# Kernel optimization log

Measured on AMD Instinct MI355X. Metric: run time of the kernel, lower is better.

The kernel has to match this reference:

```python
import jax, jax.numpy as jnp
import numpy as np

N, E, G = 16384, 131072, 64
IN_DIM, HID, HEADS, GDIM, OUT_DIM = 256, 128, 4, 2, 2


def _glorot(key, shape):
    fan_in = shape[0]
    return jax.random.normal(key, shape, dtype=jnp.float32) / jnp.sqrt(jnp.float32(fan_in))


def gatv2_layer(x, src, dst, Wl, bl, Wr, br, att, bias, heads, ch, concat):
    """GATv2Conv: e_ij = att . leaky_relu(Wl x_j + Wr x_i, 0.2), segment softmax over dst."""
    n = x.shape[0]
    xl = (x @ Wl + bl).reshape(n, heads, ch)  # source transform
    xr = (x @ Wr + br).reshape(n, heads, ch)  # target transform
    h = jax.nn.leaky_relu(xl[src] + xr[dst], 0.2)          # [E', H, C]
    e = jnp.einsum('ehc,hc->eh', h, att)                   # [E', H]
    m = jax.ops.segment_max(e, dst, num_segments=n)        # stable softmax per target
    p = jnp.exp(e - m[dst])
    denom = jax.ops.segment_sum(p, dst, num_segments=n)
    alpha = p / denom[dst]                                 # self-loops guarantee denom>0
    out = jax.ops.segment_sum(alpha[..., None] * xl[src], dst, num_segments=n)  # [n,H,C]
    out = out.reshape(n, heads * ch) if concat else out.mean(axis=1)
    return out + bias


def setup_inputs() -> dict:
    key = jax.random.key(0)
    ks = jax.random.split(key, 24)
    inp = {
        'x': jax.random.normal(ks[0], (N, IN_DIM), dtype=jnp.float32),
        'edge_index': jax.random.randint(ks[1], (2, E), 0, N, dtype=jnp.int64)
            if jax.config.jax_enable_x64 else jax.random.randint(ks[1], (2, E), 0, N).astype(jnp.int32),
        'batch': jnp.sort(jax.random.randint(ks[2], (N,), 0, G)).astype(jnp.int32),
        'global_features': jax.random.normal(ks[3], (G, GDIM), dtype=jnp.float32),
    }
    # conv1: in=256 -> heads*hid=512 (concat)
    inp['c1_Wl'] = _glorot(ks[4], (IN_DIM, HEADS * HID)); inp['c1_bl'] = jnp.zeros((HEADS * HID,), jnp.float32)
    inp['c1_Wr'] = _glorot(ks[5], (IN_DIM, HEADS * HID)); inp['c1_br'] = jnp.zeros((HEADS * HID,), jnp.float32)
    inp['c1_att'] = _glorot(ks[6], (HEADS, HID)); inp['c1_bias'] = jnp.zeros((HEADS * HID,), jnp.float32)
    # conv2: in=512 -> 512 (concat)
    D2 = HEADS * HID
    inp['c2_Wl'] = _glorot(ks[7], (D2, HEADS * HID)); inp['c2_bl'] = jnp.zeros((HEADS * HID,), jnp.float32)
    inp['c2_Wr'] = _glorot(ks[8], (D2, HEADS * HID)); inp['c2_br'] = jnp.zeros((HEADS * HID,), jnp.float32)
    inp['c2_att'] = _glorot(ks[9], (HEADS, HID)); inp['c2_bias'] = jnp.zeros((HEADS * HID,), jnp.float32)
    # conv3: in=512 -> 128 (heads=1, concat=False)
    inp['c3_Wl'] = _glorot(ks[10], (D2, HID)); inp['c3_bl'] = jnp.zeros((HID,), jnp.float32)
    inp['c3_Wr'] = _glorot(ks[11], (D2, HID)); inp['c3_br'] = jnp.zeros((HID,), jnp.float32)
    inp['c3_att'] = _glorot(ks[12], (1, HID)); inp['c3_bias'] = jnp.zeros((HID,), jnp.float32)
    # classifier: (hid + global_dim) -> hid -> out
    inp['cls_W1'] = _glorot(ks[13], (HID + GDIM, HID)); inp['cls_b1'] = jnp.zeros((HID,), jnp.float32)
    inp['cls_W2'] = _glorot(ks[14], (HID, OUT_DIM)); inp['cls_b2'] = jnp.zeros((OUT_DIM,), jnp.float32)
    return inp


def reference(x, edge_index, batch, global_features,
              c1_Wl, c1_bl, c1_Wr, c1_br, c1_att, c1_bias,
              c2_Wl, c2_bl, c2_Wr, c2_br, c2_att, c2_bias,
              c3_Wl, c3_bl, c3_Wr, c3_br, c3_att, c3_bias,
              cls_W1, cls_b1, cls_W2, cls_b2):
    n = x.shape[0]
    # PyG GATv2Conv add_self_loops=True default
    loop = jnp.arange(n, dtype=edge_index.dtype)
    src = jnp.concatenate([edge_index[0], loop])
    dst = jnp.concatenate([edge_index[1], loop])

    h = jax.nn.leaky_relu(gatv2_layer(x, src, dst, c1_Wl, c1_bl, c1_Wr, c1_br, c1_att, c1_bias, HEADS, HID, True), 0.01)
    h = jax.nn.leaky_relu(gatv2_layer(h, src, dst, c2_Wl, c2_bl, c2_Wr, c2_br, c2_att, c2_bias, HEADS, HID, True), 0.01)
    h = jax.nn.leaky_relu(gatv2_layer(h, src, dst, c3_Wl, c3_bl, c3_Wr, c3_br, c3_att, c3_bias, 1, HID, False), 0.01)

    # global mean pool over graphs
    counts = jax.ops.segment_sum(jnp.ones((n,), h.dtype), batch, num_segments=G)
    pooled = jax.ops.segment_sum(h, batch, num_segments=G) / jnp.maximum(counts, 1.0)[:, None]

    z = jnp.concatenate([pooled, global_features.reshape(G, -1)], axis=-1)
    z = jax.nn.leaky_relu(z @ cls_W1 + cls_b1, 0.01)  # Dropout is identity at eval
    return z @ cls_W2 + cls_b2
```

## Files before the change

kernel.cpp:

```cpp
#include <hip/hip_runtime.h>

typedef _Float16 h16;
typedef _Float16 h16x8 __attribute__((ext_vector_type(8)));
typedef float    f32x4 __attribute__((ext_vector_type(4)));

#define ELLW 40

__device__ __forceinline__ void gload16(const h16* g, h16* l) {
    __builtin_amdgcn_global_load_lds(
        (const __attribute__((address_space(1))) void*)g,
        (__attribute__((address_space(3))) void*)l,
        16, 0, 0);
}

__global__ __launch_bounds__(256) void prep(
    const float* __restrict__ W0, const float* __restrict__ W1,
    const float* __restrict__ W2, const float* __restrict__ W3,
    const float* __restrict__ W4, const float* __restrict__ W5,
    h16* __restrict__ O0, h16* __restrict__ O1, h16* __restrict__ O2,
    h16* __restrict__ O3, h16* __restrict__ O4, h16* __restrict__ O5,
    const float* __restrict__ x, h16* __restrict__ xh,
    int* __restrict__ cursor,
    const int* __restrict__ batch, int* __restrict__ start,
    float* __restrict__ pooled, int Nn, int G)
{
    __shared__ float lds[32][33];
    const int b = blockIdx.x;
    if (b < 896) {
        int mtx, t0;
        if      (b < 128) { mtx = 0; t0 = 0;   }
        else if (b < 256) { mtx = 1; t0 = 128; }
        else if (b < 512) { mtx = 2; t0 = 256; }
        else if (b < 768) { mtx = 3; t0 = 512; }
        else if (b < 832) { mtx = 4; t0 = 768; }
        else              { mtx = 5; t0 = 832; }
        const float* Ws[6] = {W0, W1, W2, W3, W4, W5};
        h16*         Os[6] = {O0, O1, O2, O3, O4, O5};
        const int    Ks[6] = {256, 256, 512, 512, 512, 512};
        const int    Ns[6] = {512, 512, 512, 512, 128, 128};
        const float* W = Ws[mtx];
        h16*         O = Os[mtx];
        const int K = Ks[mtx], N = Ns[mtx];
        const int tile = b - t0;
        const int tk = tile / (N >> 5), tn = tile % (N >> 5);
        const int t = threadIdx.x;
        const int r = t >> 3, c4 = (t & 7) * 4;
        float4 v = *(const float4*)(W + (size_t)(tk * 32 + r) * N + tn * 32 + c4);
        lds[r][c4] = v.x; lds[r][c4 + 1] = v.y; lds[r][c4 + 2] = v.z; lds[r][c4 + 3] = v.w;
        __syncthreads();
        h16* po = O + (size_t)(tn * 32 + r) * K + tk * 32 + c4;
        po[0] = (h16)lds[c4 + 0][r];
        po[1] = (h16)lds[c4 + 1][r];
        po[2] = (h16)lds[c4 + 2][r];
        po[3] = (h16)lds[c4 + 3][r];
        return;
    }
    int i = (b - 896) * 256 + threadIdx.x;
    const int n_x = Nn * 32;
    if (i < n_x) {
        float4 a = *(const float4*)(x + (size_t)i * 8);
        float4 c = *(const float4*)(x + (size_t)i * 8 + 4);
        h16x8 o = { (h16)a.x, (h16)a.y, (h16)a.z, (h16)a.w,
                    (h16)c.x, (h16)c.y, (h16)c.z, (h16)c.w };
        *(h16x8*)(xh + (size_t)i * 8) = o;
        return;
    }
    i -= n_x;
    if (i < Nn) { cursor[i] = 0; return; }
    i -= Nn;
    if (i < G * 128) { pooled[i] = 0.f; return; }
    i -= G * 128;
    if (i < Nn) {
        int bb = batch[i];
        int bp = (i == 0) ? -1 : batch[i - 1];
        for (int g = bp + 1; g <= bb; g++) start[g] = i;
        if (i == Nn - 1) for (int g = bb + 1; g <= G; g++) start[g] = Nn;
    }
}

__global__ void scatter_ell(const int* __restrict__ ei, int E, int Nn,
                            int* __restrict__ cursor, int* __restrict__ ssrc) {
    int i = blockIdx.x * blockDim.x + threadIdx.x;
    if (i >= E + Nn) return;
    int src, dst;
    if (i < E) { src = ei[i]; dst = ei[E + i]; }
    else       { src = dst = i - E; }
    int p = atomicAdd(&cursor[dst], 1);
    if (p < ELLW) ssrc[dst * ELLW + p] = src;
}

__device__ __forceinline__ void xcd_tiles(int& mt, int& nt) {
    int d = blockIdx.x + blockIdx.y * gridDim.x;
    int k = d & 7, j = d >> 3;
    mt = k * (gridDim.y >> 3) + j / gridDim.x;
    nt = j % gridDim.x;
}

__global__ __launch_bounds__(512) void gemm_f16_wide(
    const h16* __restrict__ Xh, const h16* __restrict__ Wt,
    const float* __restrict__ bias_lo, const float* __restrict__ bias_hi, int nsplit,
    h16* __restrict__ Yl, h16* __restrict__ Yr, int M, int N, int K)
{
    __shared__ __align__(16) h16 As[2][128 * 64];
    __shared__ __align__(16) h16 Bs[2][256 * 64];

    int mt, nt;
    xcd_tiles(mt, nt);
    const int m0 = mt * 128;
    const int n0 = nt * 256;
    const int t = threadIdx.x;
    const int lane = t & 63;
    const int wid = t >> 6;
    const int wr = wid >> 2;
    const int wc = wid & 3;

    f32x4 acc[4][4] = {};

    const int lr = lane >> 3;
    const int sl = lane & 7;

    #define STAGE(b, k0)                                                          \
        _Pragma("unroll")                                                         \
        for (int q = 0; q < 6; q++) {                                             \
            int rb = wid + 8 * q;                                                 \
            if (rb < 16) {                                                        \
                int r = rb * 8 + lr;                                              \
                int col = (sl ^ (r & 7)) << 3;                                    \
                gload16(Xh + (size_t)(m0 + r) * K + (k0) + col, &As[b][rb * 8 * 64]); \
            } else {                                                              \
                int c = (rb - 16) * 8 + lr;                                       \
                int col = (sl ^ (c & 7)) << 3;                                    \
                gload16(Wt + (size_t)(n0 + c) * K + (k0) + col, &Bs[b][(rb - 16) * 8 * 64]); \
            }                                                                     \
        }

    STAGE(0, 0)
    __syncthreads();

    const int nkb = K >> 6;
    int buf = 0;
    for (int kb = 0; kb < nkb; kb++) {
        if (kb + 1 < nkb) { STAGE(buf ^ 1, (kb + 1) << 6) }
        #pragma unroll
        for (int ks = 0; ks < 2; ks++) {
            h16x8 af[4], bf[4];
            #pragma unroll
            for (int i = 0; i < 4; i++) {
                int r  = wr * 64 + i * 16 + (lane & 15);
                int s2 = ks * 4 + (lane >> 4);
                af[i] = *(const h16x8*)(&As[buf][r * 64 + ((s2 ^ (r & 7)) << 3)]);
                int c  = wc * 64 + i * 16 + (lane & 15);
                bf[i] = *(const h16x8*)(&Bs[buf][c * 64 + ((s2 ^ (c & 7)) << 3)]);
            }
            #pragma unroll
            for (int i = 0; i < 4; i++)
                #pragma unroll
                for (int j = 0; j < 4; j++)
                    acc[i][j] = __builtin_amdgcn_mfma_f32_16x16x32_f16(af[i], bf[j], acc[i][j], 0, 0, 0);
        }
        __syncthreads();
        buf ^= 1;
    }
    #undef STAGE

    const int crow = (lane >> 4) * 4;
    const int ccol = lane & 15;
    #pragma unroll
    for (int i = 0; i < 4; i++) {
        int rg = m0 + wr * 64 + i * 16 + crow;
        #pragma unroll
        for (int j = 0; j < 4; j++) {
            int cg = n0 + wc * 64 + j * 16 + ccol;
            float b = (cg < nsplit) ? bias_lo[cg] : bias_hi[cg - nsplit];
            h16* dst = (cg < nsplit) ? (Yl + (size_t)cg) : (Yr + (size_t)(cg - nsplit));
            #pragma unroll
            for (int rr = 0; rr < 4; rr++)
                dst[(size_t)(rg + rr) * nsplit] = (h16)(acc[i][j][rr] + b);
        }
    }
}

__global__ __launch_bounds__(256) void gemm_f16_mfma(
    const h16* __restrict__ Xh, const h16* __restrict__ Wt,
    const float* __restrict__ bias_lo, const float* __restrict__ bias_hi, int nsplit,
    h16* __restrict__ Yl, h16* __restrict__ Yr, int M, int N, int K)
{
    __shared__ __align__(16) h16 As[2][128 * 64];
    __shared__ __align__(16) h16 Bs[2][128 * 64];

    int mt, nt;
    xcd_tiles(mt, nt);
    const int m0 = mt * 128;
    const int n0 = nt * 128;
    const int t = threadIdx.x;
    const int lane = t & 63;
    const int wid = t >> 6;
    const int wr = wid >> 1, wc = wid & 1;

    f32x4 acc[4][4] = {};

    const int rA = wid * 32;
    const int lr = lane >> 3;
    const int sl = lane & 7;

    #define STAGE(b, k0)                                                        \
        _Pragma("unroll")                                                       \
        for (int q = 0; q < 4; q++) {                                           \
            int rb = rA + q * 8;                                                \
            int r  = rb + lr;                                                   \
            int col = (sl ^ (r & 7)) << 3;                                      \
            gload16(Xh + (size_t)(m0 + r) * K + (k0) + col, &As[b][rb * 64]);   \
            gload16(Wt + (size_t)(n0 + r) * K + (k0) + col, &Bs[b][rb * 64]);   \
        }

    STAGE(0, 0)
    __syncthreads();

    const int nkb = K >> 6;
    int buf = 0;
    for (int kb = 0; kb < nkb; kb++) {
        if (kb + 1 < nkb) { STAGE(buf ^ 1, (kb + 1) << 6) }
        #pragma unroll
        for (int ks = 0; ks < 2; ks++) {
            h16x8 af[4], bf[4];
            #pragma unroll
            for (int i = 0; i < 4; i++) {
                int r  = wr * 64 + i * 16 + (lane & 15);
                int s2 = ks * 4 + (lane >> 4);
                af[i] = *(const h16x8*)(&As[buf][r * 64 + ((s2 ^ (r & 7)) << 3)]);
                int c  = wc * 64 + i * 16 + (lane & 15);
                bf[i] = *(const h16x8*)(&Bs[buf][c * 64 + ((s2 ^ (c & 7)) << 3)]);
            }
            #pragma unroll
            for (int i = 0; i < 4; i++)
                #pragma unroll
                for (int j = 0; j < 4; j++)
                    acc[i][j] = __builtin_amdgcn_mfma_f32_16x16x32_f16(af[i], bf[j], acc[i][j], 0, 0, 0);
        }
        __syncthreads();
        buf ^= 1;
    }
    #undef STAGE

    const int crow = (lane >> 4) * 4;
    const int ccol = lane & 15;
    #pragma unroll
    for (int i = 0; i < 4; i++) {
        int rg = m0 + wr * 64 + i * 16 + crow;
        #pragma unroll
        for (int j = 0; j < 4; j++) {
            int cg = n0 + wc * 64 + j * 16 + ccol;
            float b = (cg < nsplit) ? bias_lo[cg] : bias_hi[cg - nsplit];
            h16* dst = (cg < nsplit) ? (Yl + (size_t)cg) : (Yr + (size_t)(cg - nsplit));
            #pragma unroll
            for (int rr = 0; rr < 4; rr++)
                dst[(size_t)(rg + rr) * nsplit] = (h16)(acc[i][j][rr] + b);
        }
    }
}

template<int H, int C>
__global__ __launch_bounds__(256) void node_attn(
    const h16* __restrict__ xl, const h16* __restrict__ xr,
    const float* __restrict__ att, const float* __restrict__ bias,
    const int* __restrict__ deg, const int* __restrict__ ssrc,
    h16* __restrict__ out, int Nn)
{
    constexpr int D   = H * C;
    constexpr int EPL = D / 64;
    constexpr int LPH = C / EPL;
    int node = blockIdx.x * (blockDim.x >> 6) + (threadIdx.x >> 6);
    if (node >= Nn) return;
    const int lane = threadIdx.x & 63;
    const int base = lane * EPL;

    float xrv[EPL], attv[EPL];
    {
        h16x8 v = *(const h16x8*)(xr + (size_t)node * D + base);
        float4 a0 = *(const float4*)(att + base);
        float4 a1 = *(const float4*)(att + base + 4);
        #pragma unroll
        for (int j = 0; j < 8; j++) xrv[j] = (float)v[j];
        attv[0] = a0.x; attv[1] = a0.y; attv[2] = a0.z; attv[3] = a0.w;
        attv[4] = a1.x; attv[5] = a1.y; attv[6] = a1.z; attv[7] = a1.w;
    }

    float m = -INFINITY, denom = 0.f;
    float agg[EPL] = {};

    auto score8 = [&](h16x8 v) {
        float s = 0.f;
        #pragma unroll
        for (int j = 0; j < 8; j++) {
            float u = (float)v[j] + xrv[j];
            u = u > 0.f ? u : 0.2f * u;
            s += u * attv[j];
        }
        return s;
    };
    auto update8 = [&](float s, h16x8 v) {
        if (s > m) {
            float scale = __expf(m - s);
            denom *= scale;
            #pragma unroll
            for (int j = 0; j < 8; j++) agg[j] *= scale;
            m = s;
        }
        float p = __expf(s - m);
        denom += p;
        #pragma unroll
        for (int j = 0; j < 8; j++) agg[j] += p * (float)v[j];
    };

    const int e0 = node * ELLW, e1 = e0 + deg[node];
    int e = e0;
    for (; e + 7 < e1; e += 8) {
        int s[8];
        h16x8 xv[8];
        float sc[8];
        #pragma unroll
        for (int g = 0; g < 8; g++) s[g] = ssrc[e + g];
        #pragma unroll
        for (int g = 0; g < 8; g++) xv[g] = *(const h16x8*)(xl + (size_t)s[g] * D + base);
        #pragma unroll
        for (int g = 0; g < 8; g++) sc[g] = score8(xv[g]);
        #pragma unroll
        for (int o = 1; o < LPH; o <<= 1)
            #pragma unroll
            for (int g = 0; g < 8; g++) sc[g] += __shfl_xor(sc[g], o, 64);
        #pragma unroll
        for (int g = 0; g < 8; g++) update8(sc[g], xv[g]);
    }
    for (; e + 3 < e1; e += 4) {
        int s[4];
        h16x8 xv[4];
        float sc[4];
        #pragma unroll
        for (int g = 0; g < 4; g++) s[g] = ssrc[e + g];
        #pragma unroll
        for (int g = 0; g < 4; g++) xv[g] = *(const h16x8*)(xl + (size_t)s[g] * D + base);
        #pragma unroll
        for (int g = 0; g < 4; g++) sc[g] = score8(xv[g]);
        #pragma unroll
        for (int o = 1; o < LPH; o <<= 1)
            #pragma unroll
            for (int g = 0; g < 4; g++) sc[g] += __shfl_xor(sc[g], o, 64);
        #pragma unroll
        for (int g = 0; g < 4; g++) update8(sc[g], xv[g]);
    }
    for (; e < e1; e++) {
        int s0 = ssrc[e];
        h16x8 xa = *(const h16x8*)(xl + (size_t)s0 * D + base);
        float sc0 = score8(xa);
        #pragma unroll
        for (int o = 1; o < LPH; o <<= 1) sc0 += __shfl_xor(sc0, o, 64);
        update8(sc0, xa);
    }

    h16* po = out + (size_t)node * D + base;
    h16x8 o8;
    #pragma unroll
    for (int j = 0; j < 8; j++) {
        float v = agg[j] / denom + bias[base + j];
        o8[j] = (h16)(v > 0.f ? v : 0.01f * v);
    }
    *(h16x8*)po = o8;
}

__global__ __launch_bounds__(256) void node_attn_h1(
    const h16* __restrict__ xl, const h16* __restrict__ xr,
    const float* __restrict__ att, const float* __restrict__ bias,
    const int* __restrict__ deg, const int* __restrict__ ssrc,
    float* __restrict__ out, int Nn)
{
    int node = blockIdx.x * 4 + (threadIdx.x >> 6);
    if (node >= Nn) return;
    const int lane = threadIdx.x & 63;
    const int q    = lane >> 4;
    const int sl   = lane & 15;
    const int base = sl * 8;

    float xrv[8], attv[8];
    {
        h16x8 v = *(const h16x8*)(xr + (size_t)node * 128 + base);
        float4 a0 = *(const float4*)(att + base);
        float4 a1 = *(const float4*)(att + base + 4);
        #pragma unroll
        for (int j = 0; j < 8; j++) xrv[j] = (float)v[j];
        attv[0] = a0.x; attv[1] = a0.y; attv[2] = a0.z; attv[3] = a0.w;
        attv[4] = a1.x; attv[5] = a1.y; attv[6] = a1.z; attv[7] = a1.w;
    }

    float m = -1e30f, denom = 0.f;
    float agg[8] = {};

    const int e0 = node * ELLW, e1 = e0 + deg[node];
    for (int e = e0 + q; e < e1; e += 4) {
        int src = ssrc[e];
        h16x8 v = *(const h16x8*)(xl + (size_t)src * 128 + base);
        float s = 0.f;
        #pragma unroll
        for (int j = 0; j < 8; j++) {
            float u = (float)v[j] + xrv[j];
            u = u > 0.f ? u : 0.2f * u;
            s += u * attv[j];
        }
        #pragma unroll
        for (int o = 1; o < 16; o <<= 1) s += __shfl_xor(s, o, 64);
        if (s > m) {
            float sc = __expf(m - s);
            denom *= sc;
            #pragma unroll
            for (int j = 0; j < 8; j++) agg[j] *= sc;
            m = s;
        }
        float p = __expf(s - m);
        denom += p;
        #pragma unroll
        for (int j = 0; j < 8; j++) agg[j] += p * (float)v[j];
    }

    #pragma unroll
    for (int o = 16; o <= 32; o <<= 1) {
        float m2 = __shfl_xor(m, o, 64);
        float d2 = __shfl_xor(denom, o, 64);
        float a2[8];
        #pragma unroll
        for (int j = 0; j < 8; j++) a2[j] = __shfl_xor(agg[j], o, 64);
        float mn = fmaxf(m, m2);
        float sa = __expf(m - mn), sb = __expf(m2 - mn);
        denom = denom * sa + d2 * sb;
        #pragma unroll
        for (int j = 0; j < 8; j++) agg[j] = agg[j] * sa + a2[j] * sb;
        m = mn;
    }

    if (lane < 16) {
        float* po = out + (size_t)node * 128 + base;
        #pragma unroll
        for (int j = 0; j < 8; j++) {
            float v = agg[j] / denom + bias[base + j];
            po[j] = v > 0.f ? v : 0.01f * v;
        }
    }
}

__global__ __launch_bounds__(128) void pool_partial(
    const float* __restrict__ h, const int* __restrict__ batch,
    float* __restrict__ pooled, int Nn, int spb)
{
    int t = threadIdx.x;
    int n0 = blockIdx.x * spb;
    int n1 = min(n0 + spb, Nn);
    if (n0 >= n1) return;
    int cur = batch[n0];
    float acc = 0.f;
    for (int n = n0; n < n1; n++) {
        int g = batch[n];
        if (g != cur) {
            atomicAdd(&pooled[cur * 128 + t], acc);
            acc = 0.f; cur = g;
        }
        acc += h[(size_t)n * 128 + t];
    }
    atomicAdd(&pooled[cur * 128 + t], acc);
}

__global__ __launch_bounds__(128) void classifier(
    const float* __restrict__ pooled, const int* __restrict__ start,
    const float* __restrict__ gf,
    const float* __restrict__ W1, const float* __restrict__ b1,
    const float* __restrict__ W2, const float* __restrict__ b2,
    float* __restrict__ out)
{
    __shared__ float z[130];
    __shared__ float hid[128];
    int g = blockIdx.x, t = threadIdx.x;
    float cnt = fmaxf((float)(start[g + 1] - start[g]), 1.f);
    z[t] = pooled[g * 128 + t] / cnt;
    if (t < 2) z[128 + t] = gf[g * 2 + t];
    __syncthreads();
    float s = b1[t];
    for (int k = 0; k < 130; k++) s += z[k] * W1[k * 128 + t];
    hid[t] = s > 0.f ? s : 0.01f * s;
    __syncthreads();
    if (t < 2) {
        float o = b2[t];
        for (int j = 0; j < 128; j++) o += hid[j] * W2[j * 2 + t];
        out[g * 2 + t] = o;
    }
}

static inline int cdiv(int a, int b) { return (a + b - 1) / b; }

extern "C" void kernel_launch(void* const* d_in, const int* in_sizes, int n_in,
                              void* d_out, int out_size, void* d_ws, size_t ws_size,
                              hipStream_t stream)
{
    const float* x     = (const float*)d_in[0];
    const int*   ei    = (const int*)d_in[1];
    const int*   batch = (const int*)d_in[2];
    const float* gf    = (const float*)d_in[3];

    const float* c_Wl[3]   = {(const float*)d_in[4],  (const float*)d_in[10], (const float*)d_in[16]};
    const float* c_bl[3]   = {(const float*)d_in[5],  (const float*)d_in[11], (const float*)d_in[17]};
    const float* c_Wr[3]   = {(const float*)d_in[6],  (const float*)d_in[12], (const float*)d_in[18]};
    const float* c_br[3]   = {(const float*)d_in[7],  (const float*)d_in[13], (const float*)d_in[19]};
    const float* c_att[3]  = {(const float*)d_in[8],  (const float*)d_in[14], (const float*)d_in[20]};
    const float* c_bias[3] = {(const float*)d_in[9],  (const float*)d_in[15], (const float*)d_in[21]};
    const float* W1 = (const float*)d_in[22];
    const float* b1 = (const float*)d_in[23];
    const float* W2 = (const float*)d_in[24];
    const float* b2 = (const float*)d_in[25];
    float* out = (float*)d_out;

    const int Nn   = in_sizes[0] / 256;
    const int E    = in_sizes[1] / 2;
    const int G    = in_sizes[3] / 2;
    const int Etot = E + Nn;

    char* w = (char*)d_ws;
    auto carve = [&](size_t bytes) { void* p = w; w += (bytes + 255) & ~(size_t)255; return p; };
    h16*   ylb  = (h16*)carve((size_t)Nn * 512 * 2);
    h16*   yrb  = (h16*)carve((size_t)Nn * 512 * 2);
    h16*   xh   = (h16*)carve((size_t)Nn * 512 * 2);
    float* b0   = (float*)carve((size_t)Nn * 128 * 4);
    h16* wt1 = (h16*)carve((size_t)1024 * 256 * 2);
    h16* wt2 = (h16*)carve((size_t)1024 * 512 * 2);
    h16* wt3 = (h16*)carve((size_t)256 * 512 * 2);
    int* cursor = (int*)carve((size_t)Nn * 4);
    int* ssrc   = (int*)carve((size_t)Nn * ELLW * 4);
    int* start  = (int*)carve((size_t)(G + 1) * 4);
    float* pooled = (float*)carve((size_t)G * 128 * 4);
    (void)ws_size; (void)n_in; (void)out_size;

    {
        const int flat = Nn * 32 + Nn + G * 128 + Nn;
        prep<<<896 + cdiv(flat, 256), 256, 0, stream>>>(
            c_Wl[0], c_Wr[0], c_Wl[1], c_Wr[1], c_Wl[2], c_Wr[2],
            wt1, wt1 + 512 * 256, wt2, wt2 + 512 * 512, wt3, wt3 + 128 * 512,
            x, xh, cursor, batch, start, pooled, Nn, G);
    }
    scatter_ell<<<cdiv(Etot, 256), 256, 0, stream>>>(ei, E, Nn, cursor, ssrc);

    const int node_blocks = cdiv(Nn, 4);

    gemm_f16_wide<<<dim3(1024 / 256, Nn / 128), 512, 0, stream>>>(xh, wt1, c_bl[0], c_br[0], 512, ylb, yrb, Nn, 1024, 256);
    node_attn<4, 128><<<node_blocks, 256, 0, stream>>>(ylb, yrb, c_att[0], c_bias[0], cursor, ssrc, xh, Nn);
    gemm_f16_wide<<<dim3(1024 / 256, Nn / 128), 512, 0, stream>>>(xh, wt2, c_bl[1], c_br[1], 512, ylb, yrb, Nn, 1024, 512);
    node_attn<4, 128><<<node_blocks, 256, 0, stream>>>(ylb, yrb, c_att[1], c_bias[1], cursor, ssrc, xh, Nn);
    gemm_f16_mfma<<<dim3(256 / 128, Nn / 128), 256, 0, stream>>>(xh, wt3, c_bl[2], c_br[2], 128, ylb, yrb, Nn, 256, 512);
    node_attn_h1<<<node_blocks, 256, 0, stream>>>(ylb, yrb, c_att[2], c_bias[2], cursor, ssrc, b0, Nn);

    {
        const int nblk = 256;
        const int spb  = cdiv(Nn, nblk);
        pool_partial<<<nblk, 128, 0, stream>>>(b0, batch, pooled, Nn, spb);
    }
    classifier<<<G, 128, 0, stream>>>(pooled, start, gf, W1, b1, W2, b2, out);
}
```

Measured before the change: 190.0 us.

## Single-buffer GEMM LDS tiles and store layer-3 output as fp16

The GEMM drops its double-buffered LDS staging. Each k-step now loads its tile, syncs, computes and syncs again, which halves LDS use and may allow more resident blocks per CU, but global-load latency no longer overlaps with the MFMA work. Separately, the final attention layer writes its output in fp16 instead of fp32, and the pooling kernel reads it as fp16, which halves that buffer's traffic at a small cost in precision.

```diff
diff --git a/kernel.cpp b/kernel.cpp
--- a/kernel.cpp
+++ b/kernel.cpp
@@ -101,8 +101,8 @@
     const float* __restrict__ bias_lo, const float* __restrict__ bias_hi, int nsplit,
     h16* __restrict__ Yl, h16* __restrict__ Yr, int M, int N, int K)
 {
-    __shared__ __align__(16) h16 As[2][128 * 64];
-    __shared__ __align__(16) h16 Bs[2][256 * 64];
+    __shared__ __align__(16) h16 As[128 * 64];
+    __shared__ __align__(16) h16 Bs[256 * 64];
 
     int mt, nt;
     xcd_tiles(mt, nt);
@@ -119,28 +119,23 @@
     const int lr = lane >> 3;
     const int sl = lane & 7;
 
-    #define STAGE(b, k0)                                                          \
-        _Pragma("unroll")                                                         \
-        for (int q = 0; q < 6; q++) {                                             \
-            int rb = wid + 8 * q;                                                 \
-            if (rb < 16) {                                                        \
-                int r = rb * 8 + lr;                                              \
-                int col = (sl ^ (r & 7)) << 3;                                    \
-                gload16(Xh + (size_t)(m0 + r) * K + (k0) + col, &As[b][rb * 8 * 64]); \
-            } else {                                                              \
-                int c = (rb - 16) * 8 + lr;                                       \
-                int col = (sl ^ (c & 7)) << 3;                                    \
-                gload16(Wt + (size_t)(n0 + c) * K + (k0) + col, &Bs[b][(rb - 16) * 8 * 64]); \
-            }                                                                     \
-        }
-
-    STAGE(0, 0)
-    __syncthreads();
-
     const int nkb = K >> 6;
-    int buf = 0;
     for (int kb = 0; kb < nkb; kb++) {
-        if (kb + 1 < nkb) { STAGE(buf ^ 1, (kb + 1) << 6) }
+        const int k0 = kb << 6;
+        #pragma unroll
+        for (int q = 0; q < 6; q++) {
+            int rb = wid + 8 * q;
+            if (rb < 16) {
+                int r = rb * 8 + lr;
+                int col = (sl ^ (r & 7)) << 3;
+                gload16(Xh + (size_t)(m0 + r) * K + k0 + col, &As[rb * 8 * 64]);
+            } else {
+                int c = (rb - 16) * 8 + lr;
+                int col = (sl ^ (c & 7)) << 3;
+                gload16(Wt + (size_t)(n0 + c) * K + k0 + col, &Bs[(rb - 16) * 8 * 64]);
+            }
+        }
+        __syncthreads();
         #pragma unroll
         for (int ks = 0; ks < 2; ks++) {
             h16x8 af[4], bf[4];
@@ -148,9 +143,9 @@
             for (int i = 0; i < 4; i++) {
                 int r  = wr * 64 + i * 16 + (lane & 15);
                 int s2 = ks * 4 + (lane >> 4);
-                af[i] = *(const h16x8*)(&As[buf][r * 64 + ((s2 ^ (r & 7)) << 3)]);
+                af[i] = *(const h16x8*)(&As[r * 64 + ((s2 ^ (r & 7)) << 3)]);
                 int c  = wc * 64 + i * 16 + (lane & 15);
-                bf[i] = *(const h16x8*)(&Bs[buf][c * 64 + ((s2 ^ (c & 7)) << 3)]);
+                bf[i] = *(const h16x8*)(&Bs[c * 64 + ((s2 ^ (c & 7)) << 3)]);
             }
             #pragma unroll
             for (int i = 0; i < 4; i++)
@@ -159,9 +154,7 @@
                     acc[i][j] = __builtin_amdgcn_mfma_f32_16x16x32_f16(af[i], bf[j], acc[i][j], 0, 0, 0);
         }
         __syncthreads();
-        buf ^= 1;
-    }
-    #undef STAGE
+    }
 
     const int crow = (lane >> 4) * 4;
     const int ccol = lane & 15;
@@ -371,7 +364,7 @@
     const h16* __restrict__ xl, const h16* __restrict__ xr,
     const float* __restrict__ att, const float* __restrict__ bias,
     const int* __restrict__ deg, const int* __restrict__ ssrc,
-    float* __restrict__ out, int Nn)
+    h16* __restrict__ out, int Nn)
 {
     int node = blockIdx.x * 4 + (threadIdx.x >> 6);
     if (node >= Nn) return;
@@ -436,17 +429,19 @@
     }
 
     if (lane < 16) {
-        float* po = out + (size_t)node * 128 + base;
+        h16* po = out + (size_t)node * 128 + base;
+        h16x8 o8;
         #pragma unroll
         for (int j = 0; j < 8; j++) {
             float v = agg[j] / denom + bias[base + j];
-            po[j] = v > 0.f ? v : 0.01f * v;
-        }
+            o8[j] = (h16)(v > 0.f ? v : 0.01f * v);
+        }
+        *(h16x8*)po = o8;
     }
 }
 
 __global__ __launch_bounds__(128) void pool_partial(
-    const float* __restrict__ h, const int* __restrict__ batch,
+    const h16* __restrict__ h, const int* __restrict__ batch,
     float* __restrict__ pooled, int Nn, int spb)
 {
     int t = threadIdx.x;
@@ -461,7 +456,7 @@
             atomicAdd(&pooled[cur * 128 + t], acc);
             acc = 0.f; cur = g;
         }
-        acc += h[(size_t)n * 128 + t];
+        acc += (float)h[(size_t)n * 128 + t];
     }
     atomicAdd(&pooled[cur * 128 + t], acc);
 }
@@ -524,7 +519,7 @@
     h16*   ylb  = (h16*)carve((size_t)Nn * 512 * 2);
     h16*   yrb  = (h16*)carve((size_t)Nn * 512 * 2);
     h16*   xh   = (h16*)carve((size_t)Nn * 512 * 2);
-    float* b0   = (float*)carve((size_t)Nn * 128 * 4);
+    h16*   b0   = (h16*)carve((size_t)Nn * 128 * 2);
     h16* wt1 = (h16*)carve((size_t)1024 * 256 * 2);
     h16* wt2 = (h16*)carve((size_t)1024 * 512 * 2);
     h16* wt3 = (h16*)carve((size_t)256 * 512 * 2);
```

Measured after the change: 185.1 us (median of 2 runs). 2.6% less time.
